# Performance work log

Measured on AMD Instinct MI355X. Metric: run time of the kernel, lower is better.

The kernel has to match this reference:

```python
import jax, jax.numpy as jnp
import numpy as np


def setup_inputs() -> dict:
    key = jax.random.key(0)
    ks = jax.random.split(key, 10)
    B, C, N, W, H = 8, 512, 4096, 64, 64
    s = 1.0 / np.sqrt(C)
    return {
        "feat0": jax.random.normal(ks[0], (B, C, N), jnp.float32),
        "feat1": jax.random.normal(ks[1], (B, C, W, H), jnp.float32),
        "Wq": jax.random.normal(ks[2], (C, C), jnp.float32) * s,
        "bq": jax.random.normal(ks[3], (C,), jnp.float32) * 0.01,
        "Wk": jax.random.normal(ks[4], (C, C), jnp.float32) * s,
        "bk": jax.random.normal(ks[5], (C,), jnp.float32) * 0.01,
        "Wv": jax.random.normal(ks[6], (C, C), jnp.float32) * s,
        "bv": jax.random.normal(ks[7], (C,), jnp.float32) * 0.01,
        "Wo": jax.random.normal(ks[8], (C, C), jnp.float32) * s,
        "bo": jax.random.normal(ks[9], (C,), jnp.float32) * 0.01,
    }


def reference(feat0, feat1, Wq, bq, Wk, bk, Wv, bv, Wo, bo):
    # feat0: [B,C,N] queries; feat1: [B,C,W,H] keys/values
    B, C, N = feat0.shape
    x_q = jnp.transpose(feat0, (0, 2, 1))            # [B,N,C]
    x_kv = feat1.reshape(B, C, -1).transpose(0, 2, 1)  # [B,WH,C]

    q = x_q @ Wq.T + bq                               # [B,N,C]
    k = x_kv @ Wk.T + bk                              # [B,WH,C]
    v = x_kv @ Wv.T + bv                              # [B,WH,C]

    energy = jnp.einsum('bnc,bmc->bnm', q, k)         # [B,N,WH]
    # unconventional: softmax first, then divide by sqrt(C)
    attn = jax.nn.softmax(energy, axis=-1) * (C ** -0.5)

    ctx = jnp.einsum('bnm,bmc->bnc', attn, v)         # [B,N,C]
    out = ctx @ Wo.T + bo                             # [B,N,C]
    out = jnp.transpose(out, (0, 2, 1)) + feat0       # [B,C,N] residual
    return out
```

## Files before the change

kernel.cpp:

```cpp
#include <hip/hip_runtime.h>

#define AS1 __attribute__((address_space(1)))
#define AS3 __attribute__((address_space(3)))

typedef __bf16 bf16;
typedef unsigned char u8;
typedef unsigned int u32;
typedef __bf16 bf16x8 __attribute__((ext_vector_type(8)));
typedef __bf16 bf16x4v __attribute__((ext_vector_type(4)));
typedef float  f32x4  __attribute__((ext_vector_type(4)));
typedef long   i64x2  __attribute__((ext_vector_type(2)));

#define MFMA16(a,b,c) __builtin_amdgcn_mfma_f32_16x16x32_bf16((a),(b),(c),0,0,0)
#define MFMAF8(a,b,c) __builtin_amdgcn_mfma_f32_16x16x32_fp8_fp8((a),(b),(c),0,0,0)
#define BARX() asm volatile("s_waitcnt lgkmcnt(0)\ns_barrier" ::: "memory")
#define VMW(n) asm volatile("s_waitcnt vmcnt(" #n ")" ::: "memory")

static __device__ __forceinline__ void gll16(const bf16* src, bf16* lds) {
  __builtin_amdgcn_global_load_lds((const AS1 void*)src, (AS3 void*)lds, 16, 0, 0);
}
static __device__ __forceinline__ void gll16b(const u8* src, u8* lds) {
  __builtin_amdgcn_global_load_lds((const AS1 void*)src, (AS3 void*)lds, 16, 0, 0);
}

__global__ void convw_k(const float* __restrict__ s0, const float* __restrict__ s1,
                        const float* __restrict__ s2, const float* __restrict__ s3,
                        bf16* __restrict__ d) {
  const int which = blockIdx.x >> 8;
  const float* s = (which == 0) ? s0 : (which == 1) ? s1 : (which == 2) ? s2 : s3;
  bf16* dd = d + ((size_t)which << 18);
  int i = ((blockIdx.x & 255) * 256 + threadIdx.x) * 4;
  float4 v = *(const float4*)(s + i);
  bf16x4v o;
  o[0] = (bf16)v.x; o[1] = (bf16)v.y; o[2] = (bf16)v.z; o[3] = (bf16)v.w;
  *(bf16x4v*)(dd + i) = o;
}

__global__ void tconv_k(const float* __restrict__ f0, const float* __restrict__ f1,
                        bf16* __restrict__ xq, bf16* __restrict__ xkv) {
  const int z = blockIdx.z;
  const int b = z & 7;
  const float* src = (z < 8) ? f0 : f1;
  bf16* dst = (z < 8) ? xq : xkv;
  const int n0 = blockIdx.x * 32, c0 = blockIdx.y * 32;
  __shared__ float tile[32][33];
  const int tx = threadIdx.x, ty = threadIdx.y;
  const size_t base = (size_t)b * 512 * 4096;
#pragma unroll
  for (int i = 0; i < 4; i++) {
    int c = ty + i * 8;
    tile[c][tx] = src[base + (size_t)(c0 + c) * 4096 + n0 + tx];
  }
  __syncthreads();
  const size_t ob = (size_t)b * 4096 * 512;
#pragma unroll
  for (int i = 0; i < 4; i++) {
    int n = ty + i * 8;
    dst[ob + (size_t)(n0 + n) * 512 + c0 + tx] = (bf16)tile[tx][n];
  }
}

template<int MODE>
__global__ __launch_bounds__(256) void gemm_k(const bf16* __restrict__ A, const bf16* __restrict__ W,
                                              const float* __restrict__ bias, bf16* __restrict__ outB,
                                              float* __restrict__ outF, const float* __restrict__ resid) {
  const int b = blockIdx.y;
  const int rt = blockIdx.x >> 2, ct = blockIdx.x & 3;
  const int r0 = rt * 128, c0 = ct * 128;
  const int t = threadIdx.x, w = t >> 6, l = t & 63;
  __shared__ alignas(16) bf16 As[128 * 32];
  __shared__ alignas(16) bf16 Bs[128 * 32];
  f32x4 acc[4][4];
  const f32x4 fzero = {0.f, 0.f, 0.f, 0.f};
#pragma unroll
  for (int m = 0; m < 4; m++)
#pragma unroll
    for (int n = 0; n < 4; n++) acc[m][n] = fzero;
  const bf16* Ab = A + (size_t)b * 4096 * 512 + (size_t)r0 * 512;
  const int wr = (w >> 1) * 64, wc = (w & 1) * 64;
  for (int kk = 0; kk < 16; kk++) {
    const int k0 = kk * 32;
#pragma unroll
    for (int h = 0; h < 2; h++) {
      const int rowbase = w * 32 + h * 16;
      const int row = rowbase + (l >> 2);
      const int cl = (l & 3) ^ ((row >> 1) & 3);
      gll16(Ab + (size_t)row * 512 + k0 + cl * 8, As + rowbase * 32);
      gll16(W + (size_t)(c0 + row) * 512 + k0 + cl * 8, Bs + rowbase * 32);
    }
    __syncthreads();
    bf16x8 af[4], bfr[4];
#pragma unroll
    for (int m = 0; m < 4; m++) {
      const int row = wr + m * 16 + (l & 15);
      af[m] = *(const bf16x8*)(As + row * 32 + (((l >> 4) ^ ((row >> 1) & 3)) << 3));
    }
#pragma unroll
    for (int n = 0; n < 4; n++) {
      const int row = wc + n * 16 + (l & 15);
      bfr[n] = *(const bf16x8*)(Bs + row * 32 + (((l >> 4) ^ ((row >> 1) & 3)) << 3));
    }
#pragma unroll
    for (int m = 0; m < 4; m++)
#pragma unroll
      for (int n = 0; n < 4; n++)
        acc[m][n] = MFMA16(af[m], bfr[n], acc[m][n]);
    __syncthreads();
  }
#pragma unroll
  for (int n = 0; n < 4; n++) {
    const int co = c0 + wc + n * 16 + (l & 15);
    const float bv = bias[co];
#pragma unroll
    for (int m = 0; m < 4; m++) {
      const int rb = r0 + wr + m * 16 + ((l >> 4) << 2);
      if constexpr (MODE == 0) {
#pragma unroll
        for (int i = 0; i < 4; i++)
          outB[(size_t)b * 4096 * 512 + (size_t)(rb + i) * 512 + co] = (bf16)(acc[m][n][i] + bv);
      } else if constexpr (MODE == 1) {
        int pw = 0;
        pw = __builtin_amdgcn_cvt_pk_fp8_f32(acc[m][n][0] + bv, acc[m][n][1] + bv, pw, false);
        pw = __builtin_amdgcn_cvt_pk_fp8_f32(acc[m][n][2] + bv, acc[m][n][3] + bv, pw, true);
        const int kvin = rb & 31;
        u8* ov = (u8*)outB;
        const size_t o = (((size_t)b * 128 + (rb >> 5)) * 4 + (kvin >> 3)) * 4096 +
                         (co >> 5) * 256 + (co & 15) * 16 + ((co >> 4) & 1) * 8 + (rb & 7);
        *(int*)(ov + o) = pw;
      } else {
        const size_t o = ((size_t)b * 512 + co) * 4096 + rb;
        float4 rv = *(const float4*)(resid + o);
        float4 ov;
        ov.x = acc[m][n][0] + bv + rv.x;
        ov.y = acc[m][n][1] + bv + rv.y;
        ov.z = acc[m][n][2] + bv + rv.z;
        ov.w = acc[m][n][3] + bv + rv.w;
        *(float4*)(outF + o) = ov;
      }
    }
  }
}

__global__ __launch_bounds__(512, 2) void flash_k(const bf16* __restrict__ Q, const bf16* __restrict__ K,
                                                  const u8* __restrict__ Vt, bf16* __restrict__ ctx) {
  __shared__ alignas(16) bf16 Ks[3][32 * 512];
  __shared__ alignas(16) u8   Vs[3][16384];
  const int flat = blockIdx.x;
  const int fs = (flat & 7) * 32 + (flat >> 3);
  const int b = fs >> 5, n0 = (fs & 31) * 128;
  const int tid = threadIdx.x, w = tid >> 6, l = tid & 63;
  const int g = l >> 4, r16 = l & 15;
  const int kswz = r16 & 7;

  bf16x8 qf[16];
  {
    const bf16* Qb = Q + ((size_t)b * 4096 + n0 + w * 16 + r16) * 512 + g * 8;
#pragma unroll
    for (int f = 0; f < 16; f++) qf[f] = *(const bf16x8*)(Qb + f * 32);
  }
  f32x4 acc[32];
  const f32x4 fz = {0.f, 0.f, 0.f, 0.f};
#pragma unroll
  for (int f = 0; f < 32; f++) acc[f] = fz;
  float mrow = -1e30f, lrow = 0.f;

  int koff[4];
#pragma unroll
  for (int j = 0; j < 4; j++) {
    const int row = w * 4 + j;
    koff[j] = row * 512 + ((l ^ (row & 7)) << 3);
  }
  const int voff0 = w * 2048 + l * 16;
  const bf16* Kg = K + (size_t)b * 4096 * 512;
  const u8* Vg = Vt + (size_t)b * 128 * 16384;
  VMW(0);

#pragma unroll
  for (int j = 0; j < 4; j++) gll16(Kg + koff[j], &Ks[0][0] + (w * 4 + j) * 512);
#pragma unroll
  for (int j = 0; j < 2; j++) gll16b(Vg + voff0 + j * 1024, &Vs[0][0] + voff0 + j * 1024);

  int cur = 0, nxt = 1;
#pragma unroll 1
  for (int t = 0; t < 128; ++t) {
    if (t < 127) {
      const bf16* ks = Kg + (size_t)(t + 1) * 16384;
      const u8* vs = Vg + (size_t)(t + 1) * 16384;
      bf16* kd = &Ks[nxt][0];
      u8* vd = &Vs[nxt][0];
#pragma unroll
      for (int j = 0; j < 4; j++) gll16(ks + koff[j], kd + (w * 4 + j) * 512);
#pragma unroll
      for (int j = 0; j < 2; j++) gll16b(vs + voff0 + j * 1024, vd + voff0 + j * 1024);
      VMW(6);
    } else {
      VMW(0);
    }
    BARX();

    const bf16* kb0 = &Ks[cur][0] + r16 * 512;
    f32x4 sa = fz, sb = fz, sc2 = fz, sd = fz;
#pragma unroll
    for (int f2 = 0; f2 < 16; f2 += 2) {
      const int c0i = ((((f2 << 2) + g) ^ kswz) << 3);
      const int c1i = (((((f2 + 1) << 2) + g) ^ kswz) << 3);
      bf16x8 k0 = *(const bf16x8*)(kb0 + c0i);
      bf16x8 k1 = *(const bf16x8*)(kb0 + 16 * 512 + c0i);
      bf16x8 k2 = *(const bf16x8*)(kb0 + c1i);
      bf16x8 k3 = *(const bf16x8*)(kb0 + 16 * 512 + c1i);
      sa = MFMA16(k0, qf[f2], sa);
      sb = MFMA16(k1, qf[f2], sb);
      sc2 = MFMA16(k2, qf[f2 + 1], sc2);
      sd = MFMA16(k3, qf[f2 + 1], sd);
    }
    const f32x4 s0 = sa + sc2, s1 = sb + sd;

    float pmax = fmaxf(fmaxf(fmaxf(s0[0], s0[1]), fmaxf(s0[2], s0[3])),
                       fmaxf(fmaxf(s1[0], s1[1]), fmaxf(s1[2], s1[3])));
    pmax = fmaxf(pmax, __shfl_xor(pmax, 16));
    pmax = fmaxf(pmax, __shfl_xor(pmax, 32));
    if (!__all(pmax <= mrow + 5.0f)) {
      const float mnew = fmaxf(mrow, pmax);
      const float scl = __expf(mrow - mnew);
      mrow = mnew;
      lrow *= scl;
      const int sclI = __float_as_int(scl);
      f32x4 sc4;
#pragma unroll
      for (int i = 0; i < 4; i++)
        sc4[i] = __int_as_float(__builtin_amdgcn_ds_bpermute(((g << 2) + i) << 2, sclI));
#pragma unroll
      for (int f = 0; f < 32; f++) acc[f] *= sc4;
    }
    float p0[4], p1[4];
#pragma unroll
    for (int i = 0; i < 4; i++) { p0[i] = __expf(s0[i] - mrow); p1[i] = __expf(s1[i] - mrow); }
    float rs = (p0[0] + p0[1]) + (p0[2] + p0[3]) + (p1[0] + p1[1]) + (p1[2] + p1[3]);
    rs += __shfl_xor(rs, 16);
    rs += __shfl_xor(rs, 32);
    lrow += rs;

    int w0 = 0, w1 = 0;
    w0 = __builtin_amdgcn_cvt_pk_fp8_f32(p0[0], p0[1], w0, false);
    w0 = __builtin_amdgcn_cvt_pk_fp8_f32(p0[2], p0[3], w0, true);
    w1 = __builtin_amdgcn_cvt_pk_fp8_f32(p1[0], p1[1], w1, false);
    w1 = __builtin_amdgcn_cvt_pk_fp8_f32(p1[2], p1[3], w1, true);
    const int addrA = (((g & 1) << 5) + r16) << 2;
    const int addrB = addrA + 64;
    const int a0 = __builtin_amdgcn_ds_bpermute(addrA, w0);
    const int b0 = __builtin_amdgcn_ds_bpermute(addrB, w0);
    const int a1 = __builtin_amdgcn_ds_bpermute(addrA, w1);
    const int b1 = __builtin_amdgcn_ds_bpermute(addrB, w1);
    const bool lo2 = (g < 2);
    const u32 pA = (u32)(lo2 ? a0 : a1);
    const u32 pB = (u32)(lo2 ? b0 : b1);
    const long pf = (long)(((unsigned long long)pB << 32) | pA);

    const u8* vb = &Vs[cur][0] + g * 4096 + r16 * 16;
    __builtin_amdgcn_s_setprio(1);
#pragma unroll
    for (int c2 = 0; c2 < 16; c2++) {
      const i64x2 vv = *(const i64x2*)(vb + c2 * 256);
      acc[2 * c2] = MFMAF8(pf, vv[0], acc[2 * c2]);
      acc[2 * c2 + 1] = MFMAF8(pf, vv[1], acc[2 * c2 + 1]);
    }
    __builtin_amdgcn_s_setprio(0);
    cur = nxt;
    nxt = (nxt == 2) ? 0 : nxt + 1;
  }

  const float inv = 0.04419417382415922f / lrow;
  const int invI = __float_as_int(inv);
  float fin[4];
#pragma unroll
  for (int i = 0; i < 4; i++)
    fin[i] = __int_as_float(__builtin_amdgcn_ds_bpermute(((g << 2) + i) << 2, invI));
  const size_t ob = (size_t)b * 4096 * 512;
#pragma unroll
  for (int ct = 0; ct < 32; ct++) {
    const int c = (ct << 4) + r16;
#pragma unroll
    for (int i = 0; i < 4; i++) {
      const int n = n0 + w * 16 + (g << 2) + i;
      ctx[ob + (size_t)n * 512 + c] = (bf16)(acc[ct][i] * fin[i]);
    }
  }
}

extern "C" void kernel_launch(void* const* d_in, const int* in_sizes, int n_in,
                              void* d_out, int out_size, void* d_ws, size_t ws_size,
                              hipStream_t stream) {
  const float* feat0 = (const float*)d_in[0];
  const float* feat1 = (const float*)d_in[1];
  const float* Wq = (const float*)d_in[2];
  const float* bq = (const float*)d_in[3];
  const float* Wk = (const float*)d_in[4];
  const float* bk = (const float*)d_in[5];
  const float* Wv = (const float*)d_in[6];
  const float* bv = (const float*)d_in[7];
  const float* Wo = (const float*)d_in[8];
  const float* bo = (const float*)d_in[9];
  float* out = (float*)d_out;

  char* ws = (char*)d_ws;
  bf16* Wqb = (bf16*)(ws);
  bf16* Wkb = (bf16*)(ws + (1 << 19));
  bf16* Wvb = (bf16*)(ws + 2 * (size_t)(1 << 19));
  bf16* Wob = (bf16*)(ws + 3 * (size_t)(1 << 19));
  const size_t TEN = (size_t)8 * 4096 * 512 * 2;
  char* p = ws + 4 * (size_t)(1 << 19);
  bf16* Xq  = (bf16*)(p);
  bf16* Xkv = (bf16*)(p + TEN);
  bf16* Qb  = (bf16*)(p + 2 * TEN);
  bf16* Kb  = (bf16*)(p + 3 * TEN);
  bf16* Vtb = (bf16*)(p + 4 * TEN);
  bf16* ctx = Xq;

  convw_k<<<1024, 256, 0, stream>>>(Wq, Wk, Wv, Wo, Wqb);
  tconv_k<<<dim3(128, 16, 16), dim3(32, 8), 0, stream>>>(feat0, feat1, Xq, Xkv);
  gemm_k<0><<<dim3(128, 8), 256, 0, stream>>>(Xq,  Wqb, bq, Qb,  nullptr, nullptr);
  gemm_k<0><<<dim3(128, 8), 256, 0, stream>>>(Xkv, Wkb, bk, Kb,  nullptr, nullptr);
  gemm_k<1><<<dim3(128, 8), 256, 0, stream>>>(Xkv, Wvb, bv, Vtb, nullptr, nullptr);
  flash_k<<<dim3(256), dim3(512), 0, stream>>>(Qb, Kb, (const u8*)Vtb, ctx);
  gemm_k<2><<<dim3(128, 8), 256, 0, stream>>>(ctx, Wob, bo, nullptr, out, feat0);
}
```

Before: 469.4 us.

## Fuse K and V projections into one GEMM and defer row-sum reductions

Merges the K and V projection GEMMs into a single launch with 1024 output columns, relying on Wk and Wv being contiguous in the workspace. The first half writes bf16 K and the second half writes fp8 transposed V, so Xkv is read in one pass and one launch is saved. In the flash kernel, the cross-lane max shuffles now run only inside the rare rescale branch, and the per-iteration row-sum shuffles are deferred to one reduction at the end. This trims shuffle traffic per tile but relies on each lane's partial sums combining correctly after rescales.

```diff
diff --git a/kernel.cpp b/kernel.cpp
--- a/kernel.cpp
+++ b/kernel.cpp
@@ -65,7 +65,8 @@
                                               const float* __restrict__ bias, bf16* __restrict__ outB,
                                               float* __restrict__ outF, const float* __restrict__ resid) {
   const int b = blockIdx.y;
-  const int rt = blockIdx.x >> 2, ct = blockIdx.x & 3;
+  const int CTB = (MODE == 4) ? 3 : 2;
+  const int rt = blockIdx.x >> CTB, ct = blockIdx.x & ((1 << CTB) - 1);
   const int r0 = rt * 128, c0 = ct * 128;
   const int t = threadIdx.x, w = t >> 6, l = t & 63;
   __shared__ alignas(16) bf16 As[128 * 32];
@@ -110,7 +111,7 @@
 #pragma unroll
   for (int n = 0; n < 4; n++) {
     const int co = c0 + wc + n * 16 + (l & 15);
-    const float bv = bias[co];
+    const float bv = (MODE == 4 && co >= 512) ? resid[co - 512] : bias[co];
 #pragma unroll
     for (int m = 0; m < 4; m++) {
       const int rb = r0 + wr + m * 16 + ((l >> 4) << 2);
@@ -118,15 +119,22 @@
 #pragma unroll
         for (int i = 0; i < 4; i++)
           outB[(size_t)b * 4096 * 512 + (size_t)(rb + i) * 512 + co] = (bf16)(acc[m][n][i] + bv);
-      } else if constexpr (MODE == 1) {
-        int pw = 0;
-        pw = __builtin_amdgcn_cvt_pk_fp8_f32(acc[m][n][0] + bv, acc[m][n][1] + bv, pw, false);
-        pw = __builtin_amdgcn_cvt_pk_fp8_f32(acc[m][n][2] + bv, acc[m][n][3] + bv, pw, true);
-        const int kvin = rb & 31;
-        u8* ov = (u8*)outB;
-        const size_t o = (((size_t)b * 128 + (rb >> 5)) * 4 + (kvin >> 3)) * 4096 +
-                         (co >> 5) * 256 + (co & 15) * 16 + ((co >> 4) & 1) * 8 + (rb & 7);
-        *(int*)(ov + o) = pw;
+      } else if constexpr (MODE == 4) {
+        if (co < 512) {
+#pragma unroll
+          for (int i = 0; i < 4; i++)
+            outB[(size_t)b * 4096 * 512 + (size_t)(rb + i) * 512 + co] = (bf16)(acc[m][n][i] + bv);
+        } else {
+          const int cop = co - 512;
+          int pw = 0;
+          pw = __builtin_amdgcn_cvt_pk_fp8_f32(acc[m][n][0] + bv, acc[m][n][1] + bv, pw, false);
+          pw = __builtin_amdgcn_cvt_pk_fp8_f32(acc[m][n][2] + bv, acc[m][n][3] + bv, pw, true);
+          const int kvin = rb & 31;
+          u8* ov = (u8*)outF;
+          const size_t o = (((size_t)b * 128 + (rb >> 5)) * 4 + (kvin >> 3)) * 4096 +
+                           (cop >> 5) * 256 + (cop & 15) * 16 + ((cop >> 4) & 1) * 8 + (rb & 7);
+          *(int*)(ov + o) = pw;
+        }
       } else {
         const size_t o = ((size_t)b * 512 + co) * 4096 + rb;
         float4 rv = *(const float4*)(resid + o);
@@ -217,10 +225,10 @@
 
     float pmax = fmaxf(fmaxf(fmaxf(s0[0], s0[1]), fmaxf(s0[2], s0[3])),
                        fmaxf(fmaxf(s1[0], s1[1]), fmaxf(s1[2], s1[3])));
-    pmax = fmaxf(pmax, __shfl_xor(pmax, 16));
-    pmax = fmaxf(pmax, __shfl_xor(pmax, 32));
     if (!__all(pmax <= mrow + 5.0f)) {
-      const float mnew = fmaxf(mrow, pmax);
+      float rmax = fmaxf(pmax, __shfl_xor(pmax, 16));
+      rmax = fmaxf(rmax, __shfl_xor(rmax, 32));
+      const float mnew = fmaxf(mrow, rmax);
       const float scl = __expf(mrow - mnew);
       mrow = mnew;
       lrow *= scl;
@@ -235,10 +243,7 @@
     float p0[4], p1[4];
 #pragma unroll
     for (int i = 0; i < 4; i++) { p0[i] = __expf(s0[i] - mrow); p1[i] = __expf(s1[i] - mrow); }
-    float rs = (p0[0] + p0[1]) + (p0[2] + p0[3]) + (p1[0] + p1[1]) + (p1[2] + p1[3]);
-    rs += __shfl_xor(rs, 16);
-    rs += __shfl_xor(rs, 32);
-    lrow += rs;
+    lrow += (p0[0] + p0[1]) + (p0[2] + p0[3]) + (p1[0] + p1[1]) + (p1[2] + p1[3]);
 
     int w0 = 0, w1 = 0;
     w0 = __builtin_amdgcn_cvt_pk_fp8_f32(p0[0], p0[1], w0, false);
@@ -269,7 +274,10 @@
     nxt = (nxt == 2) ? 0 : nxt + 1;
   }
 
-  const float inv = 0.04419417382415922f / lrow;
+  float lr = lrow;
+  lr += __shfl_xor(lr, 16);
+  lr += __shfl_xor(lr, 32);
+  const float inv = 0.04419417382415922f / lr;
   const int invI = __float_as_int(inv);
   float fin[4];
 #pragma unroll
@@ -305,7 +313,6 @@
   char* ws = (char*)d_ws;
   bf16* Wqb = (bf16*)(ws);
   bf16* Wkb = (bf16*)(ws + (1 << 19));
-  bf16* Wvb = (bf16*)(ws + 2 * (size_t)(1 << 19));
   bf16* Wob = (bf16*)(ws + 3 * (size_t)(1 << 19));
   const size_t TEN = (size_t)8 * 4096 * 512 * 2;
   char* p = ws + 4 * (size_t)(1 << 19);
@@ -318,9 +325,8 @@
 
   convw_k<<<1024, 256, 0, stream>>>(Wq, Wk, Wv, Wo, Wqb);
   tconv_k<<<dim3(128, 16, 16), dim3(32, 8), 0, stream>>>(feat0, feat1, Xq, Xkv);
-  gemm_k<0><<<dim3(128, 8), 256, 0, stream>>>(Xq,  Wqb, bq, Qb,  nullptr, nullptr);
-  gemm_k<0><<<dim3(128, 8), 256, 0, stream>>>(Xkv, Wkb, bk, Kb,  nullptr, nullptr);
-  gemm_k<1><<<dim3(128, 8), 256, 0, stream>>>(Xkv, Wvb, bv, Vtb, nullptr, nullptr);
+  gemm_k<0><<<dim3(128, 8), 256, 0, stream>>>(Xq,  Wqb, bq, Qb, nullptr, nullptr);
+  gemm_k<4><<<dim3(256, 8), 256, 0, stream>>>(Xkv, Wkb, bk, Kb, (float*)Vtb, bv);
   flash_k<<<dim3(256), dim3(512), 0, stream>>>(Qb, Kb, (const u8*)Vtb, ctx);
   gemm_k<2><<<dim3(128, 8), 256, 0, stream>>>(ctx, Wob, bo, nullptr, out, feat0);
 }
```

After: 469.7 us (median of 2 runs). No clear change (+0.1%).
